# Kernel tuning notes

Measured on AMD Instinct MI355X. Metric: run time of the kernel, lower is better.

## Reference

```python
import jax, jax.numpy as jnp
import numpy as np

B, S, HID = 1, 2048, 4096
H, HKV, DFULL, D = 32, 8, 128, 96
GROUPS = H // HKV
SCALE = DFULL ** -0.5  # scaling uses the FULL head_dim per the source
ROPE_THETA = 10000.0


def setup_inputs() -> dict:
    key = jax.random.key(0)
    ks = jax.random.split(key, 8)
    hidden_states = jax.random.normal(ks[0], (B, S, HID), jnp.float32)
    # standard HF Llama RoPE tables over the FULL head dim
    inv_freq = 1.0 / (ROPE_THETA ** (jnp.arange(0, DFULL, 2, dtype=jnp.float32) / DFULL))
    ang = jnp.arange(S, dtype=jnp.float32)[:, None] * inv_freq[None, :]  # [S, DFULL/2]
    emb = jnp.concatenate([ang, ang], axis=-1)  # [S, DFULL]
    cos = jnp.cos(emb)[None]  # [1, S, DFULL]
    sin = jnp.sin(emb)[None]
    # per-kv-head frequency indices: lo half in [0, DFULL/2), hi half = lo + DFULL/2
    half, dh = DFULL // 2, D // 2
    idx_lo = jax.random.randint(ks[1], (HKV, dh), 0, half)
    indices = jnp.concatenate([idx_lo, idx_lo + half], axis=-1).astype(jnp.int32)  # [HKV, D]
    s = 0.02
    Wq = jax.random.normal(ks[2], (H * D, HID), jnp.float32) * s
    Wk = jax.random.normal(ks[3], (HKV * D, HID), jnp.float32) * s
    Wv = jax.random.normal(ks[4], (HKV * D, HID), jnp.float32) * s
    Wo = jax.random.normal(ks[5], (HID, H * D), jnp.float32) * s
    return {"hidden_states": hidden_states, "cos": cos, "sin": sin,
            "indices": indices, "Wq": Wq, "Wk": Wk, "Wv": Wv, "Wo": Wo}


def rotate_half(x):
    x1, x2 = jnp.split(x, 2, axis=-1)
    return jnp.concatenate([-x2, x1], axis=-1)


def reference(hidden_states, cos, sin, indices, Wq, Wk, Wv, Wo):
    b, s, _ = hidden_states.shape
    # QKV projections (no bias), reshape to [B, heads, S, D]
    q = (hidden_states @ Wq.T).reshape(b, s, H, D).transpose(0, 2, 1, 3)
    k = (hidden_states @ Wk.T).reshape(b, s, HKV, D).transpose(0, 2, 1, 3)
    v = (hidden_states @ Wv.T).reshape(b, s, HKV, D).transpose(0, 2, 1, 3)
    # indexed RoPE: gather per-kv-head frequencies from the full-dim tables
    cos_h = cos[:, :, indices].transpose(0, 2, 1, 3)  # [B, HKV, S, D]
    sin_h = sin[:, :, indices].transpose(0, 2, 1, 3)
    cos_q = jnp.repeat(cos_h, GROUPS, axis=1)  # [B, H, S, D]
    sin_q = jnp.repeat(sin_h, GROUPS, axis=1)
    q = q * cos_q + rotate_half(q) * sin_q
    k = k * cos_h + rotate_half(k) * sin_h
    # GQA: repeat kv to num_attention_heads
    k = jnp.repeat(k, GROUPS, axis=1)  # [B, H, S, D]
    v = jnp.repeat(v, GROUPS, axis=1)
    scores = jnp.einsum('bhqd,bhkd->bhqk', q, k) * SCALE
    causal = jnp.tril(jnp.ones((s, s), dtype=bool))
    scores = jnp.where(causal[None, None], scores, jnp.finfo(scores.dtype).min)
    probs = jax.nn.softmax(scores, axis=-1)
    out = jnp.einsum('bhqk,bhkd->bhqd', probs, v)  # [B, H, S, D]
    out = out.transpose(0, 2, 1, 3).reshape(b, s, H * D)
    return out @ Wo.T
```

## Files before the change

### kernel.cpp

```cpp
#include <hip/hip_runtime.h>

typedef unsigned short u16;
typedef unsigned int u32;
typedef __bf16 bf16x8 __attribute__((ext_vector_type(8)));
typedef float f32x4 __attribute__((ext_vector_type(4)));

#define SCALE_Q2 0.12751743443398106f

#define GLDS16(gp, lp)                                                        \
  __builtin_amdgcn_global_load_lds(                                           \
      (const __attribute__((address_space(1))) void*)(gp),                    \
      (__attribute__((address_space(3))) void*)(lp), 16, 0, 0)

__device__ __forceinline__ u16 f2bf(float f) {
  u32 u = __builtin_bit_cast(u32, f);
  u += 0x7fffu + ((u >> 16) & 1u);
  return (u16)(u >> 16);
}
__device__ __forceinline__ float bf2f(u16 b) {
  u32 u = ((u32)b) << 16;
  return __builtin_bit_cast(float, u);
}

__global__ __launch_bounds__(256) void cvt_all(const float* __restrict__ hs,
                                               const float* __restrict__ Wq,
                                               const float* __restrict__ Wk,
                                               const float* __restrict__ Wv,
                                               const float* __restrict__ Wo,
                                               u16* __restrict__ hsB,
                                               u16* __restrict__ wqkvB,
                                               u16* __restrict__ woB) {
  u32 b = blockIdx.x;
  const float* src;
  u16* dst;
  u32 i;
  if (b < 8192u) {
    src = hs; dst = hsB; i = b * 256u + threadIdx.x;
  } else if (b < 20480u) {
    src = Wq; dst = wqkvB; i = (b - 8192u) * 256u + threadIdx.x;
  } else if (b < 23552u) {
    src = Wk; dst = wqkvB + 3072u * 4096u; i = (b - 20480u) * 256u + threadIdx.x;
  } else if (b < 26624u) {
    src = Wv; dst = wqkvB + 3840u * 4096u; i = (b - 23552u) * 256u + threadIdx.x;
  } else {
    src = Wo; dst = woB; i = (b - 26624u) * 256u + threadIdx.x;
  }
  float4 v = ((const float4*)src)[i];
  u32 lo = (u32)f2bf(v.x) | ((u32)f2bf(v.y) << 16);
  u32 hi = (u32)f2bf(v.z) | ((u32)f2bf(v.w) << 16);
  ((uint2*)dst)[i] = make_uint2(lo, hi);
}

template <int NREP, bool BF16OUT>
__global__ __launch_bounds__(512, 2) void gemm8p(const u16* __restrict__ A,
                                                 const u16* __restrict__ B,
                                                 void* __restrict__ Cout,
                                                 int M, int N, int K) {
  constexpr int BN = NREP * 64;
  __shared__ u16 As[2 * 256 * 64];
  __shared__ u16 Bs[2 * BN * 64];
  const int tid = threadIdx.x;
  const int w = tid >> 6, lane = tid & 63, quad = lane >> 4, c16 = lane & 15;

  const int nx = gridDim.x;
  const int orig = blockIdx.y * nx + blockIdx.x;
  const int nwg = nx * gridDim.y;
  const int id = (orig & 7) * (nwg >> 3) + (orig >> 3);
  const int n0 = (id % nx) * BN, m0 = (id / nx) * 256;

  const int wm = (w & 1) * 128, wn = (w >> 1) * (NREP * 16);
  const int srow8 = lane >> 3, scg = (lane & 7) ^ srow8;
  const u16* Ag = A + (size_t)(m0 + w * 8 + srow8) * K + scg * 8;
  const u16* Bg = B + (size_t)(n0 + w * 8 + srow8) * K + scg * 8;
  const int axor = c16 & 7;

  f32x4 acc[8][NREP];
#pragma unroll
  for (int i = 0; i < 8; ++i)
#pragma unroll
    for (int j = 0; j < NREP; ++j) acc[i][j] = (f32x4){0.f, 0.f, 0.f, 0.f};

  const int NT = K >> 6;

#pragma unroll
  for (int j = 0; j < 4; ++j)
    GLDS16(Ag + (size_t)(j * 64) * K, &As[(j * 64 + w * 8) * 64]);
#pragma unroll
  for (int j = 0; j < NREP; ++j)
    GLDS16(Bg + (size_t)(j * 64) * K, &Bs[(j * 64 + w * 8) * 64]);

  for (int t = 0; t < NT; ++t) {
    const int sl = t & 1;
    const u16* as = &As[sl * (256 * 64)];
    const u16* bs = &Bs[sl * (BN * 64)];
    u16* asn = &As[(sl ^ 1) * (256 * 64)];
    u16* bsn = &Bs[(sl ^ 1) * (BN * 64)];
    const int kn = (t + 1) * 64;
    const bool pf = (t + 1 < NT);

    if (pf) {
#pragma unroll
      for (int j = 0; j < 4; ++j)
        GLDS16(Ag + (size_t)(j * 64) * K + kn, &asn[(j * 64 + w * 8) * 64]);
      asm volatile("s_waitcnt vmcnt(4)" ::: "memory");
    } else {
      asm volatile("s_waitcnt vmcnt(0)" ::: "memory");
    }
    __builtin_amdgcn_s_barrier();
    asm volatile("" ::: "memory");

    bf16x8 bfr[NREP][2];
#pragma unroll
    for (int nt = 0; nt < NREP; ++nt)
#pragma unroll
      for (int kk = 0; kk < 2; ++kk)
        bfr[nt][kk] = *(const bf16x8*)&bs[(wn + nt * 16 + c16) * 64 +
                                          (((kk * 4 + quad) ^ axor) * 8)];

#pragma unroll
    for (int ph = 0; ph < 4; ++ph) {
      bf16x8 afr[2][2];
#pragma unroll
      for (int i = 0; i < 2; ++i)
#pragma unroll
        for (int kk = 0; kk < 2; ++kk)
          afr[i][kk] = *(const bf16x8*)&as[(wm + (ph * 2 + i) * 16 + c16) * 64 +
                                            (((kk * 4 + quad) ^ axor) * 8)];
      if (ph == 1 && pf) {
#pragma unroll
        for (int j = 0; j < NREP; ++j)
          GLDS16(Bg + (size_t)(j * 64) * K + kn, &bsn[(j * 64 + w * 8) * 64]);
      }
      __builtin_amdgcn_s_setprio(1);
#pragma unroll
      for (int i = 0; i < 2; ++i)
#pragma unroll
        for (int nt = 0; nt < NREP; ++nt)
#pragma unroll
          for (int kk = 0; kk < 2; ++kk)
            acc[ph * 2 + i][nt] = __builtin_amdgcn_mfma_f32_16x16x32_bf16(
                afr[i][kk], bfr[nt][kk], acc[ph * 2 + i][nt], 0, 0, 0);
      __builtin_amdgcn_s_setprio(0);
    }
    asm volatile("" ::: "memory");
    __builtin_amdgcn_s_barrier();
  }

#pragma unroll
  for (int mt = 0; mt < 8; ++mt)
#pragma unroll
    for (int nt = 0; nt < NREP; ++nt)
#pragma unroll
      for (int r = 0; r < 4; ++r) {
        int m = m0 + wm + mt * 16 + quad * 4 + r;
        int n = n0 + wn + nt * 16 + c16;
        if (BF16OUT)
          ((u16*)Cout)[(size_t)m * N + n] = f2bf(acc[mt][nt][r]);
        else
          ((float*)Cout)[(size_t)m * N + n] = acc[mt][nt][r];
      }
}

__global__ __launch_bounds__(256) void rope_vt(const u16* __restrict__ qkv,
                                               const float* __restrict__ cosb,
                                               const float* __restrict__ sinb,
                                               const int* __restrict__ idxs,
                                               u16* __restrict__ qB,
                                               u16* __restrict__ kB,
                                               u16* __restrict__ vtB) {
  __shared__ u16 T[64 * 34];
  u32 bid = blockIdx.x;
  if (bid < 30720u) {
    u32 i = bid * 256u + threadIdx.x;
    const u32 NQ = 2048u * 32u * 96u;
    if (i < NQ) {
      u32 s = i / 3072u, rem = i % 3072u;
      u32 h = rem / 96u, d = rem % 96u;
      u32 hkv = h >> 2;
      u32 base = s * 4608u + h * 96u + d;
      float x = bf2f(qkv[base]);
      float pv = (d < 48u) ? -bf2f(qkv[base + 48u]) : bf2f(qkv[base - 48u]);
      int idx = idxs[hkv * 96u + d];
      float c = cosb[s * 128u + idx], sn = sinb[s * 128u + idx];
      qB[(h * 2048u + s) * 96u + d] = f2bf((x * c + pv * sn) * SCALE_Q2);
    } else {
      u32 j = i - NQ;
      u32 s = j / 768u, rem = j % 768u;
      u32 hkv = rem / 96u, d = rem % 96u;
      u32 base = s * 4608u + 3072u + hkv * 96u + d;
      float x = bf2f(qkv[base]);
      float pv = (d < 48u) ? -bf2f(qkv[base + 48u]) : bf2f(qkv[base - 48u]);
      int idx = idxs[hkv * 96u + d];
      float c = cosb[s * 128u + idx], sn = sinb[s * 128u + idx];
      kB[(hkv * 2048u + s) * 96u + d] = f2bf(x * c + pv * sn);
    }
  } else {
    u32 b2 = bid - 30720u;
    const int s0 = (b2 & 31) * 64, d0 = (int)(b2 >> 5) * 32;
    const int tx = threadIdx.x & 31, ty = threadIdx.x >> 5;
#pragma unroll
    for (int it = 0; it < 8; it++) {
      int row = it * 8 + ty;
      T[row * 34 + tx] = qkv[(size_t)(s0 + row) * 4608 + 3840 + d0 + tx];
    }
    __syncthreads();
    const int sx = threadIdx.x & 63, dy = threadIdx.x >> 6;
#pragma unroll
    for (int it = 0; it < 8; it++) {
      int d = it * 4 + dy;
      vtB[(size_t)(d0 + d) * 2048 + s0 + sx] = T[sx * 34 + d];
    }
  }
}

__global__ __launch_bounds__(256) void attn_kernel(const u16* __restrict__ qB,
                                                   const u16* __restrict__ kB,
                                                   const u16* __restrict__ vtB,
                                                   u16* __restrict__ aoB) {
  __shared__ u16 Ks[2][64 * 96];
  __shared__ u16 Vs[2][96 * 64];
  __shared__ u16 Ps[4 * 16 * 64];
  const int tid = threadIdx.x;
  const int w = tid >> 6, lane = tid & 63, quad = lane >> 4, c16 = lane & 15;
  const u32 id = blockIdx.x;
  const int hkv = id & 7;
  const int h = 4 * hkv + ((id >> 3) & 3);
  const int pr = id >> 5;
  u16* pw = Ps + w * (16 * 64);

  size_t voff[3];
#pragma unroll
  for (int it = 0; it < 3; it++) {
    int j = it * 256 + tid;
    int row = j >> 3, c = (j & 7) ^ (row & 7);
    voff[it] = (size_t)row * 2048 + c * 8;
  }
  const u16* kbase = kB + (size_t)hkv * 2048 * 96;
  const u16* vbase = vtB + (size_t)hkv * 96 * 2048;

  auto stage = [&](int buf, int kt) {
    const int k0 = kt * 64;
#pragma unroll
    for (int it = 0; it < 3; it++) {
      GLDS16(kbase + (size_t)k0 * 96 + (it * 256 + tid) * 8,
             &Ks[buf][(it * 256 + w * 64) * 8]);
      GLDS16(vbase + voff[it] + k0, &Vs[buf][(it * 256 + w * 64) * 8]);
    }
  };

  bf16x8 vones;
#pragma unroll
  for (int i = 0; i < 8; i++) vones[i] = (__bf16)1.0f;

  for (int ph = 0; ph < 2; ph++) {
    const int qt = ph ? (31 - pr) : pr;
    const int m_base = qt * 64 + w * 16;

    bf16x8 qf[3];
    {
      const u16* qrow = qB + ((size_t)h * 2048 + m_base + c16) * 96;
#pragma unroll
      for (int t = 0; t < 3; t++) qf[t] = *(const bf16x8*)(qrow + t * 32 + quad * 8);
    }
    f32x4 o[6], ol;
#pragma unroll
    for (int dt = 0; dt < 6; dt++) o[dt] = (f32x4){0.f, 0.f, 0.f, 0.f};
    ol = (f32x4){0.f, 0.f, 0.f, 0.f};

    stage(0, 0);
    __syncthreads();

    for (int kt = 0; kt <= qt; kt++) {
      const int cur = kt & 1;
      if (kt < qt) stage(cur ^ 1, kt + 1);

      f32x4 sacc[4];
#pragma unroll
      for (int nt = 0; nt < 4; nt++) sacc[nt] = (f32x4){0.f, 0.f, 0.f, 0.f};
      __builtin_amdgcn_s_setprio(1);
#pragma unroll
      for (int nt = 0; nt < 4; nt++)
#pragma unroll
        for (int t = 0; t < 3; t++) {
          bf16x8 kf = *(const bf16x8*)(&Ks[cur][(nt * 16 + c16) * 96 + t * 32 + quad * 8]);
          sacc[nt] = __builtin_amdgcn_mfma_f32_16x16x32_bf16(qf[t], kf, sacc[nt], 0, 0, 0);
        }
      __builtin_amdgcn_s_setprio(0);

      const int k0 = kt * 64;
      if (kt == qt) {
#pragma unroll
        for (int r = 0; r < 4; r++) {
          int row_abs = m_base + quad * 4 + r;
#pragma unroll
          for (int nt = 0; nt < 4; nt++)
            if (k0 + nt * 16 + c16 > row_abs) sacc[nt][r] = -__builtin_inff();
        }
      }

#pragma unroll
      for (int r = 0; r < 4; r++) {
        int mrow = quad * 4 + r, m7 = mrow & 7;
#pragma unroll
        for (int nt = 0; nt < 4; nt++) {
          float p = __builtin_amdgcn_exp2f(sacc[nt][r]);
          int chunk = (nt * 2 + (c16 >> 3)) ^ m7;
          pw[mrow * 64 + chunk * 8 + (c16 & 7)] =
              (u16)(__builtin_bit_cast(u32, p) >> 16);
        }
      }
      bf16x8 pf[2];
#pragma unroll
      for (int kti = 0; kti < 2; kti++) {
        int chunk = (kti * 4 + quad) ^ (c16 & 7);
        pf[kti] = *(const bf16x8*)(&pw[c16 * 64 + chunk * 8]);
      }
      __builtin_amdgcn_s_setprio(1);
#pragma unroll
      for (int kti = 0; kti < 2; kti++) {
        ol = __builtin_amdgcn_mfma_f32_16x16x32_bf16(pf[kti], vones, ol, 0, 0, 0);
#pragma unroll
        for (int dt = 0; dt < 6; dt++) {
          int row = dt * 16 + c16;
          int vch = (kti * 4 + quad) ^ (row & 7);
          bf16x8 vf = *(const bf16x8*)(&Vs[cur][row * 64 + vch * 8]);
          o[dt] = __builtin_amdgcn_mfma_f32_16x16x32_bf16(pf[kti], vf, o[dt], 0, 0, 0);
        }
      }
      __builtin_amdgcn_s_setprio(0);

      __syncthreads();
    }

#pragma unroll
    for (int r = 0; r < 4; r++) {
      float inv = 1.0f / ol[r];
      int row = m_base + quad * 4 + r;
#pragma unroll
      for (int dt = 0; dt < 6; dt++)
        aoB[(size_t)row * 3072 + h * 96 + dt * 16 + c16] = f2bf(o[dt][r] * inv);
    }
  }
}

extern "C" void kernel_launch(void* const* d_in, const int* in_sizes, int n_in,
                              void* d_out, int out_size, void* d_ws, size_t ws_size,
                              hipStream_t stream) {
  const float* hs   = (const float*)d_in[0];
  const float* cosb = (const float*)d_in[1];
  const float* sinb = (const float*)d_in[2];
  const int*   idxs = (const int*)d_in[3];
  const float* Wq   = (const float*)d_in[4];
  const float* Wk   = (const float*)d_in[5];
  const float* Wv   = (const float*)d_in[6];
  const float* Wo   = (const float*)d_in[7];
  float* out = (float*)d_out;
  char* ws = (char*)d_ws;

  u16* hsB   = (u16*)(ws);
  u16* wqkvB = (u16*)(ws + 16777216);
  u16* woB   = (u16*)(ws + 54525952);
  u16* qkvB  = (u16*)(ws + 79691776);
  u16* qB    = (u16*)(ws + 98566144);
  u16* kB    = (u16*)(ws + 111149056);
  u16* vtB   = (u16*)(ws + 114294784);
  u16* aoB   = (u16*)(ws + 117440512);

  cvt_all<<<38912, 256, 0, stream>>>(hs, Wq, Wk, Wv, Wo, hsB, wqkvB, woB);

  gemm8p<3, true><<<dim3(24, 8), 512, 0, stream>>>(hsB, wqkvB, qkvB, 2048, 4608, 4096);

  rope_vt<<<31488, 256, 0, stream>>>(qkvB, cosb, sinb, idxs, qB, kB, vtB);

  attn_kernel<<<512, 256, 0, stream>>>(qB, kB, vtB, aoB);

  gemm8p<2, false><<<dim3(32, 8), 512, 0, stream>>>(aoB, woB, out, 2048, 4096, 3072);
}
```

Before: 421.0 us.

## Fuse V transpose into QKV GEMM epilogue, add 128x128 output GEMM, tighten attention waits

The QKV GEMM epilogue now writes V columns straight into the transposed vtB layout, so the separate transpose blocks are dropped from the rope kernel. A new 256-thread 128x128-tile GEMM replaces the 256xBN kernel for the output projection, giving 512 workgroups instead of 256 to fill more CUs. The attention loop replaces __syncthreads with explicit vmcnt waits plus barriers so the next K/V tile prefetch can stay in flight. The transposed epilogue writes are strided, and the smaller tiles reuse less data per workgroup.

```diff
diff --git a/kernel.cpp b/kernel.cpp
--- a/kernel.cpp
+++ b/kernel.cpp
@@ -11,6 +11,20 @@
   __builtin_amdgcn_global_load_lds(                                           \
       (const __attribute__((address_space(1))) void*)(gp),                    \
       (__attribute__((address_space(3))) void*)(lp), 16, 0, 0)
+
+#define BARRIER()                                                             \
+  do {                                                                        \
+    asm volatile("" ::: "memory");                                            \
+    __builtin_amdgcn_s_barrier();                                             \
+    asm volatile("" ::: "memory");                                            \
+  } while (0)
+
+template <int N>
+__device__ __forceinline__ void vmwait() {
+  if constexpr (N == 0) asm volatile("s_waitcnt vmcnt(0)" ::: "memory");
+  else if constexpr (N == 4) asm volatile("s_waitcnt vmcnt(4)" ::: "memory");
+  else if constexpr (N == 6) asm volatile("s_waitcnt vmcnt(6)" ::: "memory");
+}
 
 __device__ __forceinline__ u16 f2bf(float f) {
   u32 u = __builtin_bit_cast(u32, f);
@@ -55,6 +69,7 @@
 __global__ __launch_bounds__(512, 2) void gemm8p(const u16* __restrict__ A,
                                                  const u16* __restrict__ B,
                                                  void* __restrict__ Cout,
+                                                 u16* __restrict__ vtB, int nv,
                                                  int M, int N, int K) {
   constexpr int BN = NREP * 64;
   __shared__ u16 As[2 * 256 * 64];
@@ -102,9 +117,9 @@
 #pragma unroll
       for (int j = 0; j < 4; ++j)
         GLDS16(Ag + (size_t)(j * 64) * K + kn, &asn[(j * 64 + w * 8) * 64]);
-      asm volatile("s_waitcnt vmcnt(4)" ::: "memory");
+      vmwait<4>();
     } else {
-      asm volatile("s_waitcnt vmcnt(0)" ::: "memory");
+      vmwait<0>();
     }
     __builtin_amdgcn_s_barrier();
     asm volatile("" ::: "memory");
@@ -146,10 +161,125 @@
     __builtin_amdgcn_s_barrier();
   }
 
-#pragma unroll
-  for (int mt = 0; mt < 8; ++mt)
-#pragma unroll
-    for (int nt = 0; nt < NREP; ++nt)
+  if (BF16OUT && n0 >= nv) {
+#pragma unroll
+    for (int mt = 0; mt < 8; ++mt)
+#pragma unroll
+      for (int nt = 0; nt < NREP; ++nt) {
+        int d_col = n0 - nv + wn + nt * 16 + c16;
+        int s_base = m0 + wm + mt * 16 + quad * 4;
+        u32 lo = (u32)f2bf(acc[mt][nt][0]) | ((u32)f2bf(acc[mt][nt][1]) << 16);
+        u32 hi = (u32)f2bf(acc[mt][nt][2]) | ((u32)f2bf(acc[mt][nt][3]) << 16);
+        *(uint2*)&vtB[(size_t)d_col * 2048 + s_base] = make_uint2(lo, hi);
+      }
+  } else {
+#pragma unroll
+    for (int mt = 0; mt < 8; ++mt)
+#pragma unroll
+      for (int nt = 0; nt < NREP; ++nt)
+#pragma unroll
+        for (int r = 0; r < 4; ++r) {
+          int m = m0 + wm + mt * 16 + quad * 4 + r;
+          int n = n0 + wn + nt * 16 + c16;
+          if (BF16OUT)
+            ((u16*)Cout)[(size_t)m * N + n] = f2bf(acc[mt][nt][r]);
+          else
+            ((float*)Cout)[(size_t)m * N + n] = acc[mt][nt][r];
+        }
+  }
+}
+
+template <bool BF16OUT>
+__global__ __launch_bounds__(256, 2) void gemm2b(const u16* __restrict__ A,
+                                                 const u16* __restrict__ B,
+                                                 void* __restrict__ Cout,
+                                                 int M, int N, int K) {
+  __shared__ u16 As[2 * 128 * 64];
+  __shared__ u16 Bs[2 * 128 * 64];
+  const int tid = threadIdx.x;
+  const int w = tid >> 6, lane = tid & 63, quad = lane >> 4, c16 = lane & 15;
+
+  const int nx = gridDim.x;
+  const int orig = blockIdx.y * nx + blockIdx.x;
+  const int nwg = nx * gridDim.y;
+  const int id = (orig & 7) * (nwg >> 3) + (orig >> 3);
+  const int n0 = (id % nx) * 128, m0 = (id / nx) * 128;
+
+  const int wm = (w & 1) * 64, wn = (w >> 1) * 64;
+  const int srow8 = lane >> 3, scg = (lane & 7) ^ srow8;
+  const u16* Ag = A + (size_t)(m0 + w * 8 + srow8) * K + scg * 8;
+  const u16* Bg = B + (size_t)(n0 + w * 8 + srow8) * K + scg * 8;
+  const int axor = c16 & 7;
+
+  f32x4 acc[4][4];
+#pragma unroll
+  for (int i = 0; i < 4; ++i)
+#pragma unroll
+    for (int j = 0; j < 4; ++j) acc[i][j] = (f32x4){0.f, 0.f, 0.f, 0.f};
+
+  const int NT = K >> 6;
+
+#pragma unroll
+  for (int j = 0; j < 4; ++j) {
+    GLDS16(Ag + (size_t)(j * 32) * K, &As[(j * 32 + w * 8) * 64]);
+    GLDS16(Bg + (size_t)(j * 32) * K, &Bs[(j * 32 + w * 8) * 64]);
+  }
+
+  for (int t = 0; t < NT; ++t) {
+    const int sl = t & 1;
+    const u16* as = &As[sl * (128 * 64)];
+    const u16* bs = &Bs[sl * (128 * 64)];
+    u16* asn = &As[(sl ^ 1) * (128 * 64)];
+    u16* bsn = &Bs[(sl ^ 1) * (128 * 64)];
+    const int kn = (t + 1) * 64;
+    const bool pf = (t + 1 < NT);
+
+    if (pf) {
+#pragma unroll
+      for (int j = 0; j < 4; ++j)
+        GLDS16(Ag + (size_t)(j * 32) * K + kn, &asn[(j * 32 + w * 8) * 64]);
+      vmwait<4>();
+    } else {
+      vmwait<0>();
+    }
+    __builtin_amdgcn_s_barrier();
+    asm volatile("" ::: "memory");
+
+#pragma unroll
+    for (int kk = 0; kk < 2; ++kk) {
+      bf16x8 af[4], bf[4];
+#pragma unroll
+      for (int mt = 0; mt < 4; ++mt) {
+        int row = wm + mt * 16 + c16;
+        af[mt] = *(const bf16x8*)&as[row * 64 + (((kk * 4 + quad) ^ axor) * 8)];
+      }
+#pragma unroll
+      for (int nt = 0; nt < 4; ++nt) {
+        int row = wn + nt * 16 + c16;
+        bf[nt] = *(const bf16x8*)&bs[row * 64 + (((kk * 4 + quad) ^ axor) * 8)];
+      }
+      if (kk == 0 && pf) {
+#pragma unroll
+        for (int j = 0; j < 4; ++j)
+          GLDS16(Bg + (size_t)(j * 32) * K + kn, &bsn[(j * 32 + w * 8) * 64]);
+      }
+      __builtin_amdgcn_s_setprio(1);
+#pragma unroll
+      for (int mt = 0; mt < 4; ++mt)
+#pragma unroll
+        for (int nt = 0; nt < 4; ++nt)
+          acc[mt][nt] = __builtin_amdgcn_mfma_f32_16x16x32_bf16(
+              af[mt], bf[nt], acc[mt][nt], 0, 0, 0);
+      __builtin_amdgcn_s_setprio(0);
+    }
+    asm volatile("" ::: "memory");
+    __builtin_amdgcn_s_barrier();
+  }
+
+#pragma unroll
+  for (int mt = 0; mt < 4; ++mt)
+#pragma unroll
+    for (int nt = 0; nt < 4; ++nt)
 #pragma unroll
       for (int r = 0; r < 4; ++r) {
         int m = m0 + wm + mt * 16 + quad * 4 + r;
@@ -161,55 +291,34 @@
       }
 }
 
-__global__ __launch_bounds__(256) void rope_vt(const u16* __restrict__ qkv,
-                                               const float* __restrict__ cosb,
-                                               const float* __restrict__ sinb,
-                                               const int* __restrict__ idxs,
-                                               u16* __restrict__ qB,
-                                               u16* __restrict__ kB,
-                                               u16* __restrict__ vtB) {
-  __shared__ u16 T[64 * 34];
-  u32 bid = blockIdx.x;
-  if (bid < 30720u) {
-    u32 i = bid * 256u + threadIdx.x;
-    const u32 NQ = 2048u * 32u * 96u;
-    if (i < NQ) {
-      u32 s = i / 3072u, rem = i % 3072u;
-      u32 h = rem / 96u, d = rem % 96u;
-      u32 hkv = h >> 2;
-      u32 base = s * 4608u + h * 96u + d;
-      float x = bf2f(qkv[base]);
-      float pv = (d < 48u) ? -bf2f(qkv[base + 48u]) : bf2f(qkv[base - 48u]);
-      int idx = idxs[hkv * 96u + d];
-      float c = cosb[s * 128u + idx], sn = sinb[s * 128u + idx];
-      qB[(h * 2048u + s) * 96u + d] = f2bf((x * c + pv * sn) * SCALE_Q2);
-    } else {
-      u32 j = i - NQ;
-      u32 s = j / 768u, rem = j % 768u;
-      u32 hkv = rem / 96u, d = rem % 96u;
-      u32 base = s * 4608u + 3072u + hkv * 96u + d;
-      float x = bf2f(qkv[base]);
-      float pv = (d < 48u) ? -bf2f(qkv[base + 48u]) : bf2f(qkv[base - 48u]);
-      int idx = idxs[hkv * 96u + d];
-      float c = cosb[s * 128u + idx], sn = sinb[s * 128u + idx];
-      kB[(hkv * 2048u + s) * 96u + d] = f2bf(x * c + pv * sn);
-    }
+__global__ __launch_bounds__(256) void rope_kernel(const u16* __restrict__ qkv,
+                                                   const float* __restrict__ cosb,
+                                                   const float* __restrict__ sinb,
+                                                   const int* __restrict__ idxs,
+                                                   u16* __restrict__ qB,
+                                                   u16* __restrict__ kB) {
+  u32 i = blockIdx.x * 256u + threadIdx.x;
+  const u32 NQ = 2048u * 32u * 96u;
+  if (i < NQ) {
+    u32 s = i / 3072u, rem = i % 3072u;
+    u32 h = rem / 96u, d = rem % 96u;
+    u32 hkv = h >> 2;
+    u32 base = s * 4608u + h * 96u + d;
+    float x = bf2f(qkv[base]);
+    float pv = (d < 48u) ? -bf2f(qkv[base + 48u]) : bf2f(qkv[base - 48u]);
+    int idx = idxs[hkv * 96u + d];
+    float c = cosb[s * 128u + idx], sn = sinb[s * 128u + idx];
+    qB[(h * 2048u + s) * 96u + d] = f2bf((x * c + pv * sn) * SCALE_Q2);
   } else {
-    u32 b2 = bid - 30720u;
-    const int s0 = (b2 & 31) * 64, d0 = (int)(b2 >> 5) * 32;
-    const int tx = threadIdx.x & 31, ty = threadIdx.x >> 5;
-#pragma unroll
-    for (int it = 0; it < 8; it++) {
-      int row = it * 8 + ty;
-      T[row * 34 + tx] = qkv[(size_t)(s0 + row) * 4608 + 3840 + d0 + tx];
-    }
-    __syncthreads();
-    const int sx = threadIdx.x & 63, dy = threadIdx.x >> 6;
-#pragma unroll
-    for (int it = 0; it < 8; it++) {
-      int d = it * 4 + dy;
-      vtB[(size_t)(d0 + d) * 2048 + s0 + sx] = T[sx * 34 + d];
-    }
+    u32 j = i - NQ;
+    u32 s = j / 768u, rem = j % 768u;
+    u32 hkv = rem / 96u, d = rem % 96u;
+    u32 base = s * 4608u + 3072u + hkv * 96u + d;
+    float x = bf2f(qkv[base]);
+    float pv = (d < 48u) ? -bf2f(qkv[base + 48u]) : bf2f(qkv[base - 48u]);
+    int idx = idxs[hkv * 96u + d];
+    float c = cosb[s * 128u + idx], sn = sinb[s * 128u + idx];
+    kB[(hkv * 2048u + s) * 96u + d] = f2bf(x * c + pv * sn);
   }
 }
 
@@ -268,11 +377,16 @@
     ol = (f32x4){0.f, 0.f, 0.f, 0.f};
 
     stage(0, 0);
-    __syncthreads();
 
     for (int kt = 0; kt <= qt; kt++) {
       const int cur = kt & 1;
-      if (kt < qt) stage(cur ^ 1, kt + 1);
+      if (kt < qt) {
+        stage(cur ^ 1, kt + 1);
+        vmwait<6>();
+      } else {
+        vmwait<0>();
+      }
+      BARRIER();
 
       f32x4 sacc[4];
 #pragma unroll
@@ -329,7 +443,7 @@
       }
       __builtin_amdgcn_s_setprio(0);
 
-      __syncthreads();
+      BARRIER();
     }
 
 #pragma unroll
@@ -368,11 +482,12 @@
 
   cvt_all<<<38912, 256, 0, stream>>>(hs, Wq, Wk, Wv, Wo, hsB, wqkvB, woB);
 
-  gemm8p<3, true><<<dim3(24, 8), 512, 0, stream>>>(hsB, wqkvB, qkvB, 2048, 4608, 4096);
-
-  rope_vt<<<31488, 256, 0, stream>>>(qkvB, cosb, sinb, idxs, qB, kB, vtB);
+  gemm8p<3, true><<<dim3(24, 8), 512, 0, stream>>>(hsB, wqkvB, qkvB, vtB, 3840,
+                                                   2048, 4608, 4096);
+
+  rope_kernel<<<30720, 256, 0, stream>>>(qkvB, cosb, sinb, idxs, qB, kB);
 
   attn_kernel<<<512, 256, 0, stream>>>(qB, kB, vtB, aoB);
 
-  gemm8p<2, false><<<dim3(32, 8), 512, 0, stream>>>(aoB, woB, out, 2048, 4096, 3072);
-}
+  gemm2b<false><<<dim3(32, 16), 256, 0, stream>>>(aoB, woB, out, 2048, 4096, 3072);
+}
```

Result: no change. 425.6 us (+1.1%).
